# Kernel optimization log

Hardware: AMD Instinct MI355X
Metric: run time of the kernel (lower is better)

## Reference

```python
import jax, jax.numpy as jnp
import numpy as np

K = 3  # sparsify_graph default k


def _lstm_dir(x, Wi, Wh, b, reverse):
    # x: [B, T, Hin]; Wi: [Hin, 4H]; Wh: [H, 4H]; b: [4H]
    B = x.shape[0]
    H = Wh.shape[0]
    xs = jnp.swapaxes(x, 0, 1)  # [T, B, Hin]
    if reverse:
        xs = xs[::-1]

    def step(carry, xt):
        h, c = carry
        g = xt @ Wi + h @ Wh + b
        i, f, gg, o = jnp.split(g, 4, axis=-1)  # torch gate order i,f,g,o
        c = jax.nn.sigmoid(f) * c + jax.nn.sigmoid(i) * jnp.tanh(gg)
        h = jax.nn.sigmoid(o) * jnp.tanh(c)
        return (h, c), h

    h0 = jnp.zeros((B, H), x.dtype)
    _, hs = jax.lax.scan(step, (h0, h0), xs)
    if reverse:
        hs = hs[::-1]
    return jnp.swapaxes(hs, 0, 1)  # [B, T, H]


def setup_inputs() -> dict:
    key = jax.random.key(0)
    ks = jax.random.split(key, 24)
    B, T, C, F = 16, 256, 64, 128
    GO, H = 32, 32  # gat_out, lstm hidden
    s = 0.1
    return {
        "x": jax.random.normal(ks[0], (B, T, C, F), jnp.float32),
        "spectral_w": jax.random.normal(ks[1], (C, F), jnp.float32),
        "gat_W": jax.random.normal(ks[2], (F, GO), jnp.float32) * s,
        "gat_a": jax.random.normal(ks[3], (2 * GO,), jnp.float32),
        "pool_w": jax.random.normal(ks[4], (GO, 1), jnp.float32) * s,
        "pool_b": jnp.zeros((1,), jnp.float32),
        "lstm_Wi_f": jax.random.normal(ks[5], (GO, 4 * H), jnp.float32) * s,
        "lstm_Wh_f": jax.random.normal(ks[6], (H, 4 * H), jnp.float32) * s,
        "lstm_b_f": jnp.zeros((4 * H,), jnp.float32),
        "lstm_Wi_r": jax.random.normal(ks[7], (GO, 4 * H), jnp.float32) * s,
        "lstm_Wh_r": jax.random.normal(ks[8], (H, 4 * H), jnp.float32) * s,
        "lstm_b_r": jnp.zeros((4 * H,), jnp.float32),
        "ta_W": jax.random.normal(ks[9], (2 * H, 2 * H), jnp.float32) * s,
        "ta_b": jnp.zeros((2 * H,), jnp.float32),
        "ta_v": jax.random.normal(ks[10], (2 * H,), jnp.float32) * s,
        "ln_g": jnp.ones((2 * H,), jnp.float32),
        "ln_b": jnp.zeros((2 * H,), jnp.float32),
        "fc1_w": jax.random.normal(ks[11], (2 * H, 32), jnp.float32) * s,
        "fc1_b": jnp.zeros((32,), jnp.float32),
        "fc2_w": jax.random.normal(ks[12], (32, 3), jnp.float32) * s,
        "fc2_b": jnp.zeros((3,), jnp.float32),
    }


def reference(x, spectral_w, gat_W, gat_a, pool_w, pool_b,
              lstm_Wi_f, lstm_Wh_f, lstm_b_f, lstm_Wi_r, lstm_Wh_r, lstm_b_r,
              ta_W, ta_b, ta_v, ln_g, ln_b, fc1_w, fc1_b, fc2_w, fc2_b):
    B, T, C, F = x.shape
    # SpectralWeighting: per-(channel,feature) softmaxed weights over feature dim
    x = x * jax.nn.softmax(spectral_w, axis=-1)  # [B,T,C,F]

    # compute_graph per sample: mean_t of cosine-similarity Gram over channels
    Hn = x / (jnp.linalg.norm(x, axis=-1, keepdims=True) + 1e-8)
    A = jnp.einsum('btcf,btdf->bcd', Hn, Hn) / T  # [B,C,C]

    # sparsify_graph: per-row top-(K+1), drop diagonal, symmetrize mask
    _, idx = jax.lax.top_k(A, K + 1)  # [B,C,K+1]
    topk_mask = jnp.sum(jax.nn.one_hot(idx, C, dtype=jnp.float32), axis=2) > 0  # [B,C,C]
    eye = jnp.eye(C, dtype=bool)
    topk_mask = topk_mask & ~eye
    topk_mask = topk_mask | jnp.swapaxes(topk_mask, 1, 2)
    A = jnp.where(topk_mask, A, 0.0)

    # GAT layer, vectorized over (B, T) with shared per-sample adjacency
    Wh = jnp.einsum('btcf,fo->btco', x, gat_W)  # [B,T,C,32]
    O = Wh.shape[-1]
    s1 = Wh @ gat_a[:O]  # [B,T,C]  a . Wh_i
    s2 = Wh @ gat_a[O:]  # [B,T,C]  a . Wh_j
    e = jax.nn.leaky_relu(s1[..., :, None] + s2[..., None, :], 0.2)  # [B,T,C,C]
    amask = (A > 0) | eye  # [B,C,C]
    e = jnp.where(amask[:, None], e, -1e9)
    alpha = jax.nn.softmax(e, axis=-1)  # dropout skipped (eval mode)
    gat = jax.nn.relu(jnp.einsum('btcd,btdo->btco', alpha, Wh))  # [B,T,C,32]

    # ChannelAttentionPooling: softmax over channel dim
    w = jax.nn.softmax(gat @ pool_w + pool_b, axis=2)  # [B,T,C,1]
    h = jnp.sum(gat * w, axis=2)  # [B,T,32]

    # BiLSTM
    hf = _lstm_dir(h, lstm_Wi_f, lstm_Wh_f, lstm_b_f, False)
    hr = _lstm_dir(h, lstm_Wi_r, lstm_Wh_r, lstm_b_r, True)
    h = jnp.concatenate([hf, hr], axis=-1)  # [B,T,64]

    # TemporalAttention (dropout skipped, eval mode)
    sc = (jnp.tanh(h @ ta_W + ta_b) @ ta_v) / 1.5  # [B,T]
    al = jax.nn.softmax(sc, axis=1)
    ctx = jnp.sum(h * al[..., None], axis=1)  # [B,64]

    # LayerNorm
    mu = jnp.mean(ctx, axis=-1, keepdims=True)
    var = jnp.var(ctx, axis=-1, keepdims=True)
    ctx = (ctx - mu) / jnp.sqrt(var + 1e-5) * ln_g + ln_b

    # Classifier head (dropout skipped, eval mode)
    return jax.nn.relu(ctx @ fc1_w + fc1_b) @ fc2_w + fc2_b  # [B,3]
```

## Files before the change

### kernel.cpp

```cpp
#include <hip/hip_runtime.h>
#include <hip/hip_bf16.h>

#define B_  16
#define T_  256
#define C_  64
#define F_  128
#define O_  32
#define H_  32
#define G4_ 128

typedef __attribute__((ext_vector_type(8))) short bfrag;
typedef __attribute__((ext_vector_type(4))) float f4acc;

__device__ __forceinline__ unsigned short f2bf(float v) {
    union { float f; unsigned u; } c; c.f = v;
    unsigned r = c.u + 0x7FFF + ((c.u >> 16) & 1);
    return (unsigned short)(r >> 16);
}
__device__ __forceinline__ float bf2f(unsigned short b) {
    union { float f; unsigned u; } c; c.u = ((unsigned)b) << 16; return c.f;
}
__device__ __forceinline__ float sigm_f(float x) {
    return __builtin_amdgcn_rcpf(1.f + __expf(-x));
}
__device__ __forceinline__ float tanh_f(float x) {
    float e = __expf(2.f * x);
    return 1.f - 2.f * __builtin_amdgcn_rcpf(e + 1.f);
}
__device__ __forceinline__ float readlane_f(float v, int l) {
    return __int_as_float(__builtin_amdgcn_readlane(__float_as_int(v), l));
}

__global__ __launch_bounds__(64) void k_sw(const float* __restrict__ w,
                                           float* __restrict__ sw) {
    int c = blockIdx.x, lane = threadIdx.x;
    const float* row = w + c * F_;
    float v0 = row[lane], v1 = row[lane + 64];
    float m = fmaxf(v0, v1);
#pragma unroll
    for (int s = 1; s < 64; s <<= 1) m = fmaxf(m, __shfl_xor(m, s));
    float e0 = __expf(v0 - m), e1 = __expf(v1 - m);
    float s = e0 + e1;
#pragma unroll
    for (int s_ = 1; s_ < 64; s_ <<= 1) s += __shfl_xor(s, s_);
    sw[c * F_ + lane] = e0 / s;
    sw[c * F_ + lane + 64] = e1 / s;
}

#define TCP 4
#define PSTR 136

#define MFMA16(a, b, c) __builtin_amdgcn_mfma_f32_16x16x32_bf16(a, b, c, 0, 0, 0)

__global__ __launch_bounds__(256) void k_phase1(
    const float* __restrict__ x, const float* __restrict__ sw,
    const float* __restrict__ gat_W, const float* __restrict__ gat_a,
    float* __restrict__ A, float* __restrict__ Wh,
    float* __restrict__ s1, float* __restrict__ s2) {
    const int b = blockIdx.x, tc = blockIdx.y, tid = threadIdx.x;
    const int wv = tid >> 6, lane = tid & 63;
    const int quad = lane >> 4, l16 = lane & 15;

    __shared__ unsigned short hhi[64 * PSTR];
    __shared__ unsigned short hlo[64 * PSTR];
    __shared__ float nrm[64];
    __shared__ float s1p[2][64], s2p[2][64];

    float4 swr[8];
    {
        const float4* sw4 = (const float4*)sw;
#pragma unroll
        for (int i = 0; i < 8; i++) swr[i] = sw4[tid + 256 * i];
    }

    const int rt0 = (wv >> 1) * 2;
    const int ct0 = (wv & 1) * 2;
    const int jW = wv & 1;

    bfrag wfh[4], wfl[4];
    {
        const int n = l16 + 16 * jW;
#pragma unroll
        for (int k = 0; k < 4; k++) {
            union { unsigned short u[8]; bfrag v; } Hu, Lu;
#pragma unroll
            for (int u = 0; u < 8; u++) {
                float v = gat_W[(32 * k + quad * 8 + u) * O_ + n];
                unsigned short hb = f2bf(v);
                Hu.u[u] = hb;
                Lu.u[u] = f2bf(v - bf2f(hb));
            }
            wfh[k] = Hu.v;
            wfl[k] = Lu.v;
        }
    }
    const float ga1 = gat_a[l16 + 16 * jW];
    const float ga2 = gat_a[O_ + l16 + 16 * jW];

    f4acc accA[2][2];
#pragma unroll
    for (int i = 0; i < 2; i++)
#pragma unroll
        for (int j = 0; j < 2; j++) accA[i][j] = (f4acc){0.f, 0.f, 0.f, 0.f};

    for (int tt = 0; tt < TCP; ++tt) {
        const int t = tc * TCP + tt;
        const float4* xg = (const float4*)(x + ((size_t)(b * T_ + t) << 13));
        float4 xr[8];
#pragma unroll
        for (int i = 0; i < 8; i++) xr[i] = xg[tid + 256 * i];

        __syncthreads();

        float invn_[8];
#pragma unroll
        for (int i = 0; i < 8; i++) {
            float4 v = xr[i], s = swr[i];
            v.x *= s.x; v.y *= s.y; v.z *= s.z; v.w *= s.w;
            xr[i] = v;
            float ss = v.x * v.x + v.y * v.y + v.z * v.z + v.w * v.w;
#pragma unroll
            for (int d = 1; d < 32; d <<= 1) ss += __shfl_xor(ss, d);
            float nv = sqrtf(ss) + 1e-8f;
            invn_[i] = 1.0f / nv;
            if ((tid & 31) == 0) nrm[(tid >> 5) + 8 * i] = nv;
        }
#pragma unroll
        for (int i = 0; i < 8; i++) {
            int c = (tid >> 5) + 8 * i;
            float4 v = xr[i];
            float iv = invn_[i];
            float a0 = v.x * iv, a1 = v.y * iv, a2 = v.z * iv, a3 = v.w * iv;
            union { unsigned short u[4]; unsigned long long q; } Hq, Lq;
            unsigned short h0 = f2bf(a0), h1 = f2bf(a1), h2 = f2bf(a2), h3 = f2bf(a3);
            Hq.u[0] = h0; Hq.u[1] = h1; Hq.u[2] = h2; Hq.u[3] = h3;
            Lq.u[0] = f2bf(a0 - bf2f(h0));
            Lq.u[1] = f2bf(a1 - bf2f(h1));
            Lq.u[2] = f2bf(a2 - bf2f(h2));
            Lq.u[3] = f2bf(a3 - bf2f(h3));
            int off = c * PSTR + 4 * (tid & 31);
            *(unsigned long long*)&hhi[off] = Hq.q;
            *(unsigned long long*)&hlo[off] = Lq.q;
        }
        __syncthreads();

        f4acc accW0 = (f4acc){0.f, 0.f, 0.f, 0.f};
        f4acc accW1 = (f4acc){0.f, 0.f, 0.f, 0.f};
#pragma unroll
        for (int k = 0; k < 4; k++) {
            const int ko = 32 * k + 8 * quad;
            bfrag r0h = *(const bfrag*)&hhi[(rt0 * 16 + l16) * PSTR + ko];
            bfrag r0l = *(const bfrag*)&hlo[(rt0 * 16 + l16) * PSTR + ko];
            bfrag r1h = *(const bfrag*)&hhi[((rt0 + 1) * 16 + l16) * PSTR + ko];
            bfrag r1l = *(const bfrag*)&hlo[((rt0 + 1) * 16 + l16) * PSTR + ko];
            bfrag c0h = *(const bfrag*)&hhi[(ct0 * 16 + l16) * PSTR + ko];
            bfrag c0l = *(const bfrag*)&hlo[(ct0 * 16 + l16) * PSTR + ko];
            bfrag c1h = *(const bfrag*)&hhi[((ct0 + 1) * 16 + l16) * PSTR + ko];
            bfrag c1l = *(const bfrag*)&hlo[((ct0 + 1) * 16 + l16) * PSTR + ko];
            accA[0][0] = MFMA16(r0h, c0h, accA[0][0]);
            accA[0][0] = MFMA16(r0h, c0l, accA[0][0]);
            accA[0][0] = MFMA16(r0l, c0h, accA[0][0]);
            accA[0][1] = MFMA16(r0h, c1h, accA[0][1]);
            accA[0][1] = MFMA16(r0h, c1l, accA[0][1]);
            accA[0][1] = MFMA16(r0l, c1h, accA[0][1]);
            accA[1][0] = MFMA16(r1h, c0h, accA[1][0]);
            accA[1][0] = MFMA16(r1h, c0l, accA[1][0]);
            accA[1][0] = MFMA16(r1l, c0h, accA[1][0]);
            accA[1][1] = MFMA16(r1h, c1h, accA[1][1]);
            accA[1][1] = MFMA16(r1h, c1l, accA[1][1]);
            accA[1][1] = MFMA16(r1l, c1h, accA[1][1]);
            accW0 = MFMA16(r0h, wfh[k], accW0);
            accW0 = MFMA16(r0h, wfl[k], accW0);
            accW0 = MFMA16(r0l, wfh[k], accW0);
            accW1 = MFMA16(r1h, wfh[k], accW1);
            accW1 = MFMA16(r1h, wfl[k], accW1);
            accW1 = MFMA16(r1l, wfh[k], accW1);
        }
        float* whout = Wh + (size_t)(b * T_ + t) * (C_ * O_);
#pragma unroll
        for (int i2 = 0; i2 < 2; i2++) {
            f4acc aw = i2 ? accW1 : accW0;
#pragma unroll
            for (int r = 0; r < 4; r++) {
                int row = (rt0 + i2) * 16 + quad * 4 + r;
                float val = aw[r] * nrm[row];
                whout[row * O_ + l16 + 16 * jW] = val;
                float v1 = val * ga1, v2 = val * ga2;
#pragma unroll
                for (int d = 1; d < 16; d <<= 1) {
                    v1 += __shfl_xor(v1, d);
                    v2 += __shfl_xor(v2, d);
                }
                if (l16 == 0) { s1p[jW][row] = v1; s2p[jW][row] = v2; }
            }
        }
        __syncthreads();
        if (tid < 64) {
            s1[(b * T_ + t) * C_ + tid] = s1p[0][tid] + s1p[1][tid];
            s2[(b * T_ + t) * C_ + tid] = s2p[0][tid] + s2p[1][tid];
        }
    }
#pragma unroll
    for (int i2 = 0; i2 < 2; i2++)
#pragma unroll
        for (int j2 = 0; j2 < 2; j2++)
#pragma unroll
            for (int r = 0; r < 4; r++) {
                int row = (rt0 + i2) * 16 + quad * 4 + r;
                int col = (ct0 + j2) * 16 + l16;
                atomicAdd(&A[b * (C_ * C_) + row * C_ + col], accA[i2][j2][r]);
            }
}

__global__ __launch_bounds__(64) void k_topk(const float* __restrict__ A,
                                             unsigned long long* __restrict__ amask) {
    int b = blockIdx.x;
    int c = threadIdx.x;
    __shared__ unsigned long long tk[C_];
    const float* row = A + b * (C_ * C_) + c * C_;
    unsigned long long sel = 0ULL;
    for (int r = 0; r < 4; r++) {
        float best = -1e30f;
        int bi = 0;
        for (int d = 0; d < C_; d++) {
            if (sel & (1ULL << d)) continue;
            float v = row[d];
            if (v > best) { best = v; bi = d; }
        }
        sel |= (1ULL << bi);
    }
    unsigned long long t = sel & ~(1ULL << c);
    tk[c] = t;
    __syncthreads();
    unsigned long long sym = t;
    for (int d = 0; d < C_; d++)
        if ((tk[d] >> c) & 1ULL) sym |= (1ULL << d);
    unsigned long long m = (1ULL << c);
    unsigned long long s2 = sym;
    while (s2) {
        int d = __ffsll(s2) - 1;
        s2 &= s2 - 1;
        if (row[d] > 0.f) m |= (1ULL << d);
    }
    amask[b * C_ + c] = m;
}

__global__ __launch_bounds__(256) void k_gat(
    const float* __restrict__ Wh, const float* __restrict__ s1,
    const float* __restrict__ s2, const unsigned long long* __restrict__ amask,
    const float* __restrict__ pool_w, const float* __restrict__ pool_b,
    float* __restrict__ hout) {
    int tg = blockIdx.x;
    int wv = threadIdx.x >> 6, c = threadIdx.x & 63;
    int bt = tg * 4 + wv;
    int b = bt >> 8;
    __shared__ float buf[4][C_][33];
    __shared__ float s2s[4][C_];

    s2s[wv][c] = s2[bt * C_ + c];
    float s1c = s1[bt * C_ + c];
    unsigned long long m = amask[b * C_ + c];
    __syncthreads();

    float mx = -1e30f;
    unsigned long long mm = m;
    while (mm) {
        int d = __ffsll(mm) - 1; mm &= mm - 1;
        float v = s1c + s2s[wv][d];
        v = v > 0.f ? v : 0.2f * v;
        mx = fmaxf(mx, v);
    }
    float ssum = 0.f;
    mm = m;
    while (mm) {
        int d = __ffsll(mm) - 1; mm &= mm - 1;
        float v = s1c + s2s[wv][d];
        v = v > 0.f ? v : 0.2f * v;
        ssum += __expf(v - mx);
    }
    float inv = 1.0f / ssum;
    float g[O_];
#pragma unroll
    for (int i = 0; i < O_; i++) g[i] = 0.f;
    mm = m;
    while (mm) {
        int d = __ffsll(mm) - 1; mm &= mm - 1;
        float v = s1c + s2s[wv][d];
        v = v > 0.f ? v : 0.2f * v;
        float a = __expf(v - mx);
        const float4* wr = (const float4*)(Wh + (size_t)bt * (C_ * O_) + d * O_);
#pragma unroll
        for (int q = 0; q < 8; q++) {
            float4 w4 = wr[q];
            g[4 * q + 0] += a * w4.x;
            g[4 * q + 1] += a * w4.y;
            g[4 * q + 2] += a * w4.z;
            g[4 * q + 3] += a * w4.w;
        }
    }
    float lg = pool_b[0];
#pragma unroll
    for (int i = 0; i < O_; i++) {
        g[i] = fmaxf(g[i] * inv, 0.f);
        lg += g[i] * pool_w[i];
    }
    float wmx = lg;
#pragma unroll
    for (int s = 1; s < 64; s <<= 1) wmx = fmaxf(wmx, __shfl_xor(wmx, s));
    float we = __expf(lg - wmx);
    float wsum = we;
#pragma unroll
    for (int s = 1; s < 64; s <<= 1) wsum += __shfl_xor(wsum, s);
    float wcf = we / wsum;
#pragma unroll
    for (int i = 0; i < O_; i++) buf[wv][c][i] = g[i] * wcf;
    __syncthreads();
    {
        int wt = threadIdx.x >> 6, o = threadIdx.x & 31, hf = (threadIdx.x >> 5) & 1;
        float sacc = 0.f;
#pragma unroll 8
        for (int d = hf * 32; d < hf * 32 + 32; d++) sacc += buf[wt][d][o];
        sacc += __shfl_xor(sacc, 32);
        if (hf == 0) hout[(tg * 4 + wt) * O_ + o] = sacc;
    }
}

__global__ __launch_bounds__(128) void k_lstm_pre(
    const float* __restrict__ hin,
    const float* __restrict__ Wi_f, const float* __restrict__ b_f,
    const float* __restrict__ Wi_r, const float* __restrict__ b_r,
    float* __restrict__ gx) {
    int id = blockIdx.x;
    int dir = id >> 12;
    int bt = id & 4095;
    const float* Wi = dir ? Wi_r : Wi_f;
    const float* bb = dir ? b_r : b_f;
    int g = threadIdx.x;
    __shared__ float hs[H_];
    if (g < H_) hs[g] = hin[bt * O_ + g];
    __syncthreads();
    float acc = bb[g];
#pragma unroll
    for (int k = 0; k < H_; k++) acc += hs[k] * Wi[k * G4_ + g];
    gx[((size_t)dir * 4096 + bt) * G4_ + g] = acc;
}

#define WW(k) float2 ww##k = make_float2(Wd[(k) * G4_ + lane], Wd[(k) * G4_ + lane + 64]);
#define KST(k, Aq) { float hk = readlane_f(h, k); \
    Aq.x = fmaf(hk, ww##k.x, Aq.x); Aq.y = fmaf(hk, ww##k.y, Aq.y); }

__global__ void __attribute__((amdgpu_flat_work_group_size(64, 64)))
__attribute__((amdgpu_waves_per_eu(1, 1))) k_lstm_seq(
    const float* __restrict__ gx,
    const float* __restrict__ Whf, const float* __restrict__ Whr,
    float* __restrict__ hcat) {
    int dir = blockIdx.x & 1, b = blockIdx.x >> 1;
    int lane = threadIdx.x;
    const float* Wd = dir ? Whr : Whf;
    WW(0) WW(1) WW(2) WW(3) WW(4) WW(5) WW(6) WW(7)
    WW(8) WW(9) WW(10) WW(11) WW(12) WW(13) WW(14) WW(15)
    WW(16) WW(17) WW(18) WW(19) WW(20) WW(21) WW(22) WW(23)
    WW(24) WW(25) WW(26) WW(27) WW(28) WW(29) WW(30) WW(31)

    const float* gxb = gx + ((size_t)dir * 4096 + b * T_) * G4_;
    float h = 0.f, cst = 0.f;
    const int dt = dir ? -1 : 1;
    int t = dir ? (T_ - 1) : 0;
    float g0n = gxb[t * G4_ + lane], g1n = gxb[t * G4_ + lane + 64];
    const float half_sel = (lane < 32) ? 2.f : 1.f;
    for (int s = 0; s < T_; s++) {
        int tn = t + dt;
        float2 A0 = make_float2(g0n, g1n);
        float2 A1 = make_float2(0.f, 0.f);
        float2 A2 = make_float2(0.f, 0.f);
        float2 A3 = make_float2(0.f, 0.f);
        if (s < T_ - 1) {
            g0n = gxb[tn * G4_ + lane];
            g1n = gxb[tn * G4_ + lane + 64];
        }
        KST(0, A0)  KST(1, A1)  KST(2, A2)  KST(3, A3)
        KST(4, A0)  KST(5, A1)  KST(6, A2)  KST(7, A3)
        KST(8, A0)  KST(9, A1)  KST(10, A2) KST(11, A3)
        KST(12, A0) KST(13, A1) KST(14, A2) KST(15, A3)
        KST(16, A0) KST(17, A1) KST(18, A2) KST(19, A3)
        KST(20, A0) KST(21, A1) KST(22, A2) KST(23, A3)
        KST(24, A0) KST(25, A1) KST(26, A2) KST(27, A3)
        KST(28, A0) KST(29, A1) KST(30, A2) KST(31, A3)
        float g0 = (A0.x + A1.x) + (A2.x + A3.x);
        float g1 = (A0.y + A1.y) + (A2.y + A3.y);
        float sA = sigm_f(g0);
        float u = sigm_f(half_sel * g1);
        float sB = (lane < 32) ? fmaf(2.f, u, -1.f) : u;
        float sf = __shfl(sA, (lane & 31) + 32);
        float so = __shfl(sB, (lane & 31) + 32);
        cst = fmaf(sf, cst, sA * sB);
        float hn = so * tanh_f(cst);
        h = hn;
        if (lane < H_) hcat[((size_t)(b * T_) + t) * (2 * H_) + dir * H_ + lane] = hn;
        t = tn;
    }
}

__global__ __launch_bounds__(256) void k_final(
    const float* __restrict__ hcat,
    const float* __restrict__ taW, const float* __restrict__ tab,
    const float* __restrict__ tav,
    const float* __restrict__ lng, const float* __restrict__ lnb,
    const float* __restrict__ w1, const float* __restrict__ b1,
    const float* __restrict__ w2, const float* __restrict__ b2,
    float* __restrict__ out) {
    int b = blockIdx.x;
    int t = threadIdx.x;
    __shared__ float Wl[64 * 64];
    __shared__ float al[T_];
    __shared__ float wred[4];
    __shared__ float ctxp[4][64];
    __shared__ float ctx[64];
    __shared__ float a1[32];
    for (int i = t; i < 4096; i += 256) Wl[i] = taW[i];
    float4 hr[16];
    const float4* hb = (const float4*)(hcat + ((size_t)b * T_ + t) * 64);
#pragma unroll
    for (int i = 0; i < 16; i++) hr[i] = hb[i];
    __syncthreads();
    float sc = 0.f;
    for (int j = 0; j < 64; j++) {
        float s = tab[j];
#pragma unroll
        for (int k4 = 0; k4 < 16; k4++) {
            float4 h4 = hr[k4];
            const float* wcol = &Wl[(4 * k4) * 64 + j];
            s += h4.x * wcol[0] + h4.y * wcol[64] + h4.z * wcol[128] + h4.w * wcol[192];
        }
        sc += tanhf(s) * tav[j];
    }
    sc *= (1.0f / 1.5f);
    int wave = t >> 6, lane = t & 63;
    float m = sc;
#pragma unroll
    for (int s_ = 1; s_ < 64; s_ <<= 1) m = fmaxf(m, __shfl_xor(m, s_));
    if (lane == 0) wred[wave] = m;
    __syncthreads();
    m = fmaxf(fmaxf(wred[0], wred[1]), fmaxf(wred[2], wred[3]));
    float e = __expf(sc - m);
    float ssum = e;
#pragma unroll
    for (int s_ = 1; s_ < 64; s_ <<= 1) ssum += __shfl_xor(ssum, s_);
    __syncthreads();
    if (lane == 0) wred[wave] = ssum;
    __syncthreads();
    float S = wred[0] + wred[1] + wred[2] + wred[3];
    al[t] = e / S;
    __syncthreads();
    {
        int o = t & 63, part = t >> 6;
        float cacc = 0.f;
        for (int tt = part * 64; tt < part * 64 + 64; tt++)
            cacc += al[tt] * hcat[((size_t)b * T_ + tt) * 64 + o];
        ctxp[part][o] = cacc;
    }
    __syncthreads();
    if (t < 64) {
        float ctxo = ctxp[0][t] + ctxp[1][t] + ctxp[2][t] + ctxp[3][t];
        float sv = ctxo, sq = ctxo * ctxo;
#pragma unroll
        for (int s_ = 1; s_ < 64; s_ <<= 1) {
            sv += __shfl_xor(sv, s_);
            sq += __shfl_xor(sq, s_);
        }
        float mu = sv * (1.f / 64.f);
        float var = sq * (1.f / 64.f) - mu * mu;
        ctx[t] = (ctxo - mu) / sqrtf(var + 1e-5f) * lng[t] + lnb[t];
    }
    __syncthreads();
    if (t < 32) {
        float s = b1[t];
        for (int k = 0; k < 64; k++) s += ctx[k] * w1[k * 32 + t];
        a1[t] = fmaxf(s, 0.f);
    }
    __syncthreads();
    if (t < 3) {
        float s = b2[t];
        for (int k = 0; k < 32; k++) s += a1[k] * w2[k * 3 + t];
        out[b * 3 + t] = s;
    }
}

extern "C" void kernel_launch(void* const* d_in, const int* in_sizes, int n_in,
                              void* d_out, int out_size, void* d_ws, size_t ws_size,
                              hipStream_t stream) {
    const float* x          = (const float*)d_in[0];
    const float* spectral_w = (const float*)d_in[1];
    const float* gat_W      = (const float*)d_in[2];
    const float* gat_a      = (const float*)d_in[3];
    const float* pool_w     = (const float*)d_in[4];
    const float* pool_b     = (const float*)d_in[5];
    const float* lstm_Wi_f  = (const float*)d_in[6];
    const float* lstm_Wh_f  = (const float*)d_in[7];
    const float* lstm_b_f   = (const float*)d_in[8];
    const float* lstm_Wi_r  = (const float*)d_in[9];
    const float* lstm_Wh_r  = (const float*)d_in[10];
    const float* lstm_b_r   = (const float*)d_in[11];
    const float* ta_W       = (const float*)d_in[12];
    const float* ta_b       = (const float*)d_in[13];
    const float* ta_v       = (const float*)d_in[14];
    const float* ln_g       = (const float*)d_in[15];
    const float* ln_b       = (const float*)d_in[16];
    const float* fc1_w      = (const float*)d_in[17];
    const float* fc1_b      = (const float*)d_in[18];
    const float* fc2_w      = (const float*)d_in[19];
    const float* fc2_b      = (const float*)d_in[20];
    float* out = (float*)d_out;

    float* ws = (float*)d_ws;
    float* sw    = ws + 0;
    float* A     = ws + 8192;
    unsigned long long* amask = (unsigned long long*)(ws + 73728);
    float* Wh    = ws + 75776;
    float* s1    = ws + 8464384;
    float* s2    = ws + 8726528;
    float* hpool = ws + 8988672;
    float* gx    = ws + 9119744;
    float* hcat  = ws + 10168320;

    hipMemsetAsync(A, 0, (size_t)C_ * C_ * B_ * sizeof(float), stream);
    k_sw<<<C_, 64, 0, stream>>>(spectral_w, sw);
    k_phase1<<<dim3(B_, T_ / TCP), 256, 0, stream>>>(x, sw, gat_W, gat_a, A, Wh, s1, s2);
    k_topk<<<B_, 64, 0, stream>>>(A, amask);
    k_gat<<<B_ * T_ / 4, 256, 0, stream>>>(Wh, s1, s2, amask, pool_w, pool_b, hpool);
    k_lstm_pre<<<2 * B_ * T_, 128, 0, stream>>>(hpool, lstm_Wi_f, lstm_b_f,
                                                lstm_Wi_r, lstm_b_r, gx);
    k_lstm_seq<<<2 * B_, 64, 0, stream>>>(gx, lstm_Wh_f, lstm_Wh_r, hcat);
    k_final<<<B_, 256, 0, stream>>>(hcat, ta_W, ta_b, ta_v, ln_g, ln_b,
                                    fc1_w, fc1_b, fc2_w, fc2_b, out);
}
```

Measured before the change: 443.2 us.

## Prefetch next timestep in phase1 and deepen LSTM gx prefetch to four steps

In k_phase1, the x load for the next timestep is issued right after the LDS barrier so it overlaps the MFMA work. This removes one __syncthreads per iteration and adds an occupancy hint to launch_bounds. In the sequential LSTM kernel, the loop is unrolled by four with a rotating four-deep register prefetch of the input-gate preactivations, hiding global load latency on the serial recurrence. The cost is higher register pressure, and the dropped barrier relies on the second barrier to keep LDS reuse safe.

```diff
diff --git a/kernel.cpp b/kernel.cpp
--- a/kernel.cpp
+++ b/kernel.cpp
@@ -52,7 +52,7 @@
 
 #define MFMA16(a, b, c) __builtin_amdgcn_mfma_f32_16x16x32_bf16(a, b, c, 0, 0, 0)
 
-__global__ __launch_bounds__(256) void k_phase1(
+__global__ __launch_bounds__(256, 4) void k_phase1(
     const float* __restrict__ x, const float* __restrict__ sw,
     const float* __restrict__ gat_W, const float* __restrict__ gat_a,
     float* __restrict__ A, float* __restrict__ Wh,
@@ -103,14 +103,16 @@
 #pragma unroll
         for (int j = 0; j < 2; j++) accA[i][j] = (f4acc){0.f, 0.f, 0.f, 0.f};
 
+    float4 xr[8];
+    {
+        const int t = tc * TCP;
+        const float4* xg = (const float4*)(x + ((size_t)(b * T_ + t) << 13));
+#pragma unroll
+        for (int i = 0; i < 8; i++) xr[i] = xg[tid + 256 * i];
+    }
+
     for (int tt = 0; tt < TCP; ++tt) {
         const int t = tc * TCP + tt;
-        const float4* xg = (const float4*)(x + ((size_t)(b * T_ + t) << 13));
-        float4 xr[8];
-#pragma unroll
-        for (int i = 0; i < 8; i++) xr[i] = xg[tid + 256 * i];
-
-        __syncthreads();
 
         float invn_[8];
 #pragma unroll
@@ -143,6 +145,13 @@
             *(unsigned long long*)&hlo[off] = Lq.q;
         }
         __syncthreads();
+
+        if (tt < TCP - 1) {
+            const float4* xg =
+                (const float4*)(x + ((size_t)(b * T_ + t + 1) << 13));
+#pragma unroll
+            for (int i = 0; i < 8; i++) xr[i] = xg[tid + 256 * i];
+        }
 
         f4acc accW0 = (f4acc){0.f, 0.f, 0.f, 0.f};
         f4acc accW1 = (f4acc){0.f, 0.f, 0.f, 0.f};
@@ -349,6 +358,38 @@
 #define KST(k, Aq) { float hk = readlane_f(h, k); \
     Aq.x = fmaf(hk, ww##k.x, Aq.x); Aq.y = fmaf(hk, ww##k.y, Aq.y); }
 
+#define LSTEP(P, SC) { \
+    float2 A0 = make_float2(P##x, P##y); \
+    float2 A1 = make_float2(0.f, 0.f); \
+    float2 A2 = make_float2(0.f, 0.f); \
+    float2 A3 = make_float2(0.f, 0.f); \
+    if ((SC) + 4 < T_) { \
+        int tn_ = dir ? (T_ - 1 - ((SC) + 4)) : ((SC) + 4); \
+        P##x = gxb[tn_ * G4_ + lane]; \
+        P##y = gxb[tn_ * G4_ + lane + 64]; \
+    } \
+    KST(0, A0)  KST(1, A1)  KST(2, A2)  KST(3, A3) \
+    KST(4, A0)  KST(5, A1)  KST(6, A2)  KST(7, A3) \
+    KST(8, A0)  KST(9, A1)  KST(10, A2) KST(11, A3) \
+    KST(12, A0) KST(13, A1) KST(14, A2) KST(15, A3) \
+    KST(16, A0) KST(17, A1) KST(18, A2) KST(19, A3) \
+    KST(20, A0) KST(21, A1) KST(22, A2) KST(23, A3) \
+    KST(24, A0) KST(25, A1) KST(26, A2) KST(27, A3) \
+    KST(28, A0) KST(29, A1) KST(30, A2) KST(31, A3) \
+    float g0 = (A0.x + A1.x) + (A2.x + A3.x); \
+    float g1 = (A0.y + A1.y) + (A2.y + A3.y); \
+    float sA = sigm_f(g0); \
+    float u = sigm_f(half_sel * g1); \
+    float sB = (lane < 32) ? fmaf(2.f, u, -1.f) : u; \
+    float sf = __shfl(sA, (lane & 31) + 32); \
+    float so = __shfl(sB, (lane & 31) + 32); \
+    cst = fmaf(sf, cst, sA * sB); \
+    float hn = so * tanh_f(cst); \
+    h = hn; \
+    { int tc_ = dir ? (T_ - 1 - (SC)) : (SC); \
+      if (lane < H_) hcat[((size_t)(b * T_) + tc_) * (2 * H_) + dir * H_ + lane] = hn; } \
+}
+
 __global__ void __attribute__((amdgpu_flat_work_group_size(64, 64)))
 __attribute__((amdgpu_waves_per_eu(1, 1))) k_lstm_seq(
     const float* __restrict__ gx,
@@ -364,40 +405,24 @@
 
     const float* gxb = gx + ((size_t)dir * 4096 + b * T_) * G4_;
     float h = 0.f, cst = 0.f;
-    const int dt = dir ? -1 : 1;
-    int t = dir ? (T_ - 1) : 0;
-    float g0n = gxb[t * G4_ + lane], g1n = gxb[t * G4_ + lane + 64];
     const float half_sel = (lane < 32) ? 2.f : 1.f;
-    for (int s = 0; s < T_; s++) {
-        int tn = t + dt;
-        float2 A0 = make_float2(g0n, g1n);
-        float2 A1 = make_float2(0.f, 0.f);
-        float2 A2 = make_float2(0.f, 0.f);
-        float2 A3 = make_float2(0.f, 0.f);
-        if (s < T_ - 1) {
-            g0n = gxb[tn * G4_ + lane];
-            g1n = gxb[tn * G4_ + lane + 64];
-        }
-        KST(0, A0)  KST(1, A1)  KST(2, A2)  KST(3, A3)
-        KST(4, A0)  KST(5, A1)  KST(6, A2)  KST(7, A3)
-        KST(8, A0)  KST(9, A1)  KST(10, A2) KST(11, A3)
-        KST(12, A0) KST(13, A1) KST(14, A2) KST(15, A3)
-        KST(16, A0) KST(17, A1) KST(18, A2) KST(19, A3)
-        KST(20, A0) KST(21, A1) KST(22, A2) KST(23, A3)
-        KST(24, A0) KST(25, A1) KST(26, A2) KST(27, A3)
-        KST(28, A0) KST(29, A1) KST(30, A2) KST(31, A3)
-        float g0 = (A0.x + A1.x) + (A2.x + A3.x);
-        float g1 = (A0.y + A1.y) + (A2.y + A3.y);
-        float sA = sigm_f(g0);
-        float u = sigm_f(half_sel * g1);
-        float sB = (lane < 32) ? fmaf(2.f, u, -1.f) : u;
-        float sf = __shfl(sA, (lane & 31) + 32);
-        float so = __shfl(sB, (lane & 31) + 32);
-        cst = fmaf(sf, cst, sA * sB);
-        float hn = so * tanh_f(cst);
-        h = hn;
-        if (lane < H_) hcat[((size_t)(b * T_) + t) * (2 * H_) + dir * H_ + lane] = hn;
-        t = tn;
+
+    float p0x, p0y, p1x, p1y, p2x, p2y, p3x, p3y;
+    {
+        int t0 = dir ? (T_ - 1) : 0;
+        int t1 = dir ? (T_ - 2) : 1;
+        int t2 = dir ? (T_ - 3) : 2;
+        int t3 = dir ? (T_ - 4) : 3;
+        p0x = gxb[t0 * G4_ + lane]; p0y = gxb[t0 * G4_ + lane + 64];
+        p1x = gxb[t1 * G4_ + lane]; p1y = gxb[t1 * G4_ + lane + 64];
+        p2x = gxb[t2 * G4_ + lane]; p2y = gxb[t2 * G4_ + lane + 64];
+        p3x = gxb[t3 * G4_ + lane]; p3y = gxb[t3 * G4_ + lane + 64];
+    }
+    for (int s = 0; s < T_; s += 4) {
+        LSTEP(p0, s + 0)
+        LSTEP(p1, s + 1)
+        LSTEP(p2, s + 2)
+        LSTEP(p3, s + 3)
     }
 }
 
```

After: 537.7 us. 21.3% more time.
